# Kernel optimization log

Measured on AMD Instinct MI355X. Metric: run time of the kernel, lower is better.

The kernel has to match this reference:

```python
import jax, jax.numpy as jnp
import numpy as np


def setup_inputs() -> dict:
    key = jax.random.key(0)
    k1, k2 = jax.random.split(key)
    z = jax.random.normal(k1, (16, 256, 4096), dtype=jnp.float32)  # (B, z_dim, T)
    embedding = jax.random.normal(k2, (1024, 256), dtype=jnp.float32)  # (z_num, z_dim)
    return {"z": z, "embedding": embedding}


def reference(z, embedding):
    # z: (B, C, T) -> (B, T, C), matching z.transpose(1, 2)
    zt = jnp.transpose(z, (0, 2, 1))
    B, T, C = zt.shape
    z_flat = zt.reshape(-1, C)  # (N, C), N = B*T

    # squared-euclidean distances: ||z||^2 + ||e||^2 - 2 z e^T  -> (N, K)
    distances = (
        jnp.sum(z_flat * z_flat, axis=1, keepdims=True)
        + jnp.sum(embedding * embedding, axis=1)
        - 2.0 * z_flat @ embedding.T
    )
    encoding_idx = jnp.argmin(distances, axis=1)  # (N,)
    z_vq = embedding[encoding_idx].reshape(B, T, C)

    # perplexity of code usage (one-hot scatter -> mean)
    K = embedding.shape[0]
    counts = jnp.zeros((K,), dtype=jnp.float32).at[encoding_idx].add(1.0)
    avg_probs = counts / encoding_idx.shape[0]
    perplexity = jnp.exp(-jnp.sum(avg_probs * jnp.log(avg_probs + 1e-10)))

    # sparsity = cross_entropy(E E^T, arange) = mean(logsumexp(row) - diag)
    logits = embedding @ embedding.T  # (K, K)
    sparsity = jnp.mean(jax.nn.logsumexp(logits, axis=1) - jnp.diag(logits))

    sg = jax.lax.stop_gradient
    z_qut_loss = jnp.sum((z_vq - sg(zt)) ** 2)   # mse_loss reduction='sum'
    z_enc_loss = jnp.sum((sg(z_vq) - zt) ** 2)

    # straight-through estimator
    z_st = zt + sg(z_vq - zt)
    out = jnp.transpose(z_st, (0, 2, 1))  # back to (B, C, T)
    return (out, z_qut_loss, z_enc_loss, perplexity, sparsity)
```

## Files before the change

kernel.cpp:

```cpp
#include <hip/hip_runtime.h>
#include <math.h>

typedef unsigned int u32;
typedef unsigned long long u64;
typedef _Float16 f16x8 __attribute__((ext_vector_type(8)));
typedef _Float16 f16x4 __attribute__((ext_vector_type(4)));
typedef float f32x4 __attribute__((ext_vector_type(4)));
typedef __attribute__((address_space(1))) const char gch;
typedef __attribute__((address_space(3))) char lch;

#define ZD 256
#define KC 1024
#define TT 4096
#define BB 16
#define NROWS (BB*TT)
#define TAU 0.12f
#define FLAGCAP 32768

__device__ __forceinline__ u32 flip32(float s) {
    int i = __float_as_int(s);
    return (u32)(i ^ ((i >> 31) | 0x80000000));
}
__device__ __forceinline__ float unflip32(u32 u) {
    int m = (~(((int)u) >> 31)) | 0x80000000;
    return __int_as_float((int)(u ^ (u32)m));
}

__global__ __launch_bounds__(256)
void vq_prep_kernel(const float* __restrict__ emb, _Float16* __restrict__ eh,
                    float* __restrict__ re, int* __restrict__ cnt) {
    int gid = blockIdx.x * 256 + threadIdx.x;
    if (gid < 2) cnt[gid] = 0;

    int code = gid >> 6;
    int lane = threadIdx.x & 63;
    float4 v = *(const float4*)(emb + (size_t)code * ZD + lane * 4);
    float s = v.x*v.x + v.y*v.y + v.z*v.z + v.w*v.w;
    #pragma unroll
    for (int off = 32; off; off >>= 1) s += __shfl_down(s, off, 64);
    if (lane == 0) re[code] = s;

    f16x4 hv;
    hv[0] = (_Float16)v.x; hv[1] = (_Float16)v.y;
    hv[2] = (_Float16)v.z; hv[3] = (_Float16)v.w;
    *(f16x4*)(eh + (size_t)code * ZD + lane * 4) = hv;
}

__device__ __forceinline__ void stage_half4(const char* ehc, char* dstbase,
                                            int h, int w, int l) {
    const int srow = h * 16384;
    #pragma unroll
    for (int j = 0; j < 4; ++j) {
        const int gi  = w * 4 + j;
        const int c   = 2 * gi + (l >> 5);
        const int kbs = (l & 31) * 16;
        const int off = srow + c * 512 + (kbs ^ ((c & 7) << 4));
        __builtin_amdgcn_global_load_lds((gch*)(ehc + off),
                                         (lch*)(dstbase + gi * 1024), 16, 0, 0);
    }
}

__device__ __forceinline__ void compute_phase32(const char* hb, int h,
                                                const f16x8 (&ah)[2][8], const float* reL,
                                                float (&v1)[8], float (&v2)[8], int (&i1)[8],
                                                int lane15, int lk) {
    #pragma unroll
    for (int cg = 0; cg < 2; ++cg) {
        const int c  = cg * 16 + lane15;
        const int sw = (lane15 & 7) << 4;
        f16x8 bh[8];
        #pragma unroll
        for (int ks = 0; ks < 8; ++ks)
            bh[ks] = *(const f16x8*)(hb + c * 512 + ((lk * 16 + ks * 64) ^ sw));

        f32x4 a0 = {0.f, 0.f, 0.f, 0.f};
        f32x4 a1 = {0.f, 0.f, 0.f, 0.f};
        __builtin_amdgcn_s_setprio(1);
        #pragma unroll
        for (int ks = 0; ks < 8; ++ks) {
            a0 = __builtin_amdgcn_mfma_f32_16x16x32_f16(ah[0][ks], bh[ks], a0, 0, 0, 0);
            a1 = __builtin_amdgcn_mfma_f32_16x16x32_f16(ah[1][ks], bh[ks], a1, 0, 0, 0);
        }
        __builtin_amdgcn_s_setprio(0);

        const int codeg = h * 32 + c;
        const float rc = reL[codeg];
        #pragma unroll
        for (int r = 0; r < 4; ++r) {
            float s0 = fmaf(-2.f, a0[r], rc);
            float n2a = fminf(fmaxf(v1[r], s0), v2[r]);
            i1[r] = (s0 < v1[r]) ? codeg : i1[r];
            v1[r] = fminf(v1[r], s0);
            v2[r] = n2a;
            float s1 = fmaf(-2.f, a1[r], rc);
            float n2b = fminf(fmaxf(v1[4 + r], s1), v2[4 + r]);
            i1[4 + r] = (s1 < v1[4 + r]) ? codeg : i1[4 + r];
            v1[4 + r] = fminf(v1[4 + r], s1);
            v2[4 + r] = n2b;
        }
    }
}

__global__ __launch_bounds__(256, 3)
void vq_argmin_mfma(const float* __restrict__ z, const _Float16* __restrict__ eh,
                    const float* __restrict__ emb, const float* __restrict__ re,
                    float* __restrict__ out, float* __restrict__ lossP,
                    int* __restrict__ idx, int* __restrict__ cnt,
                    int* __restrict__ flags) {
    __shared__ __align__(16) char lds[53248];
    float* reL    = (float*)(lds + 49152);
    int*   idsL   = (int*)lds;
    float* wlossL = (float*)(lds + 512);

    const int tid = threadIdx.x;
    const int w   = tid >> 6;
    const int l   = tid & 63;
    const int lane15 = l & 15;
    const int lk     = l >> 4;
    const int r0  = blockIdx.x * 128;
    const int b   = r0 >> 12;
    const int t0  = r0 & 4095;
    const char* ehc = (const char*)eh;

    *(float4*)(reL + tid * 4) = *(const float4*)(re + tid * 4);

    f16x8 ah[2][8];
    float zsq[2] = {0.f, 0.f};
    {
        const char* zb = (const char*)(z + (size_t)b * ZD * TT + t0 + w * 32);
        char* zdst = lds + w * 8192;
        #pragma unroll
        for (int round = 0; round < 4; ++round) {
            #pragma unroll
            for (int j = 0; j < 8; ++j) {
                const int c  = round * 64 + j * 8 + (l >> 3);
                const int tb = (l & 7) * 16;
                const char* src = zb + (size_t)c * TT * 4 + tb;
                __builtin_amdgcn_global_load_lds((gch*)src, (lch*)(zdst + j * 1024),
                                                 16, 0, 0);
            }
            asm volatile("s_waitcnt vmcnt(0)" ::: "memory");
            __builtin_amdgcn_sched_barrier(0);
            #pragma unroll
            for (int rg = 0; rg < 2; ++rg) {
                const int tw = rg * 16 + lane15;
                #pragma unroll
                for (int ks2 = 0; ks2 < 2; ++ks2) {
                    const int cl = ks2 * 32 + lk * 8;
                    f16x8 h;
                    #pragma unroll
                    for (int j = 0; j < 8; ++j) {
                        float v = *(const float*)(zdst + (cl + j) * 128 + tw * 4);
                        zsq[rg] = fmaf(v, v, zsq[rg]);
                        h[j] = (_Float16)v;
                    }
                    ah[rg][round * 2 + ks2] = h;
                }
            }
            asm volatile("s_waitcnt lgkmcnt(0)" ::: "memory");
            __builtin_amdgcn_sched_barrier(0);
        }
    }
    #pragma unroll
    for (int rg = 0; rg < 2; ++rg) {
        zsq[rg] += __shfl_xor(zsq[rg], 16, 64);
        zsq[rg] += __shfl_xor(zsq[rg], 32, 64);
    }

    float v1[8], v2[8];
    int   i1[8];
    #pragma unroll
    for (int s8 = 0; s8 < 8; ++s8) { v1[s8] = 3.4e38f; v2[s8] = 3.4e38f; i1[s8] = 0; }

    asm volatile("s_waitcnt vmcnt(0) lgkmcnt(0)" ::: "memory");
    __syncthreads();
    stage_half4(ehc, lds,         0, w, l);
    stage_half4(ehc, lds + 16384, 1, w, l);

    for (int h = 0; h < 31; ++h) {
        asm volatile("s_waitcnt vmcnt(4)" ::: "memory");
        __builtin_amdgcn_sched_barrier(0);
        __builtin_amdgcn_s_barrier();
        if (h < 30) stage_half4(ehc, lds + ((h + 2) % 3) * 16384, h + 2, w, l);
        compute_phase32(lds + (h % 3) * 16384, h, ah, reL, v1, v2, i1, lane15, lk);
    }
    asm volatile("s_waitcnt vmcnt(0)" ::: "memory");
    __builtin_amdgcn_sched_barrier(0);
    __builtin_amdgcn_s_barrier();
    compute_phase32(lds + (31 % 3) * 16384, 31, ah, reL, v1, v2, i1, lane15, lk);

    #pragma unroll
    for (int off = 1; off < 16; off <<= 1) {
        #pragma unroll
        for (int s8 = 0; s8 < 8; ++s8) {
            float ov1 = __shfl_xor(v1[s8], off, 64);
            int   oi1 = __shfl_xor(i1[s8], off, 64);
            float ov2 = __shfl_xor(v2[s8], off, 64);
            float nv2 = fminf(fmaxf(v1[s8], ov1), fminf(v2[s8], ov2));
            if (ov1 < v1[s8] || (ov1 == v1[s8] && oi1 < i1[s8])) { v1[s8] = ov1; i1[s8] = oi1; }
            v2[s8] = nv2;
        }
    }

    float zsr[8];
    #pragma unroll
    for (int s8 = 0; s8 < 8; ++s8) {
        const int rg = s8 >> 2, rr = s8 & 3;
        zsr[s8] = __shfl(zsq[rg], lk * 4 + rr, 64);
    }

    __syncthreads();
    float lossw = 0.f;
    if (lane15 == 0) {
        #pragma unroll
        for (int s8 = 0; s8 < 8; ++s8) {
            const int rg = s8 >> 2, rr = s8 & 3;
            const int row = w * 32 + rg * 16 + lk * 4 + rr;
            idsL[row] = i1[s8];
            const bool fl = (v2[s8] - v1[s8] < TAU);
            lossw += fl ? zsr[s8] : (zsr[s8] + v1[s8]);
            if (fl) {
                int p = atomicAdd(cnt, 1);
                if (p < FLAGCAP) flags[p] = (r0 + row) | (i1[s8] << 16);
            }
        }
    }
    lossw += __shfl_xor(lossw, 16, 64);
    lossw += __shfl_xor(lossw, 32, 64);
    if (l == 0) wlossL[w] = lossw;
    __syncthreads();

    if (tid < 128) idx[r0 + tid] = idsL[tid];
    if (tid == 0) lossP[blockIdx.x] = wlossL[0] + wlossL[1] + wlossL[2] + wlossL[3];

    {
        const int c0 = w * 64;
        float* ob = out + (size_t)b * ZD * TT + t0;
        #pragma unroll
        for (int half = 0; half < 2; ++half) {
            const int tt = half * 64 + l;
            const int ii = idsL[tt];
            const float4* er4 = (const float4*)(emb + (size_t)ii * ZD + c0);
            #pragma unroll
            for (int c4 = 0; c4 < 16; ++c4) {
                float4 ev = er4[c4];
                float* o0 = ob + (size_t)(c0 + c4 * 4) * TT + tt;
                o0[0]      = ev.x;
                o0[TT]     = ev.y;
                o0[2 * TT] = ev.z;
                o0[3 * TT] = ev.w;
            }
        }
    }
}

__global__ __launch_bounds__(256)
void vq_fixup_spar(const float* __restrict__ z, const float* __restrict__ emb,
                   const float* __restrict__ re, const int* __restrict__ cnt,
                   const int* __restrict__ flags, float* __restrict__ out,
                   int* __restrict__ idx, float* __restrict__ spar,
                   float* __restrict__ addP) {
    const int tid = threadIdx.x;
    const int w   = tid >> 6;
    const int lane = tid & 63;

    if (blockIdx.x >= 128) {
        __shared__ __align__(16) float er[8][260];
        __shared__ float wmaxS[8][4];
        __shared__ float wsumS[8][4];
        __shared__ float shD[8];
        const int bid2 = blockIdx.x - 128;
        const int r0   = bid2 * 8;

        for (int i = tid; i < 8 * 256; i += 256) er[i >> 8][i & 255] = emb[(size_t)r0 * ZD + i];
        __syncthreads();

        float dots[4][8];
        #pragma unroll
        for (int cc = 0; cc < 4; ++cc) {
            const int c = cc * 256 + tid;
            const float4* ec = (const float4*)(emb + (size_t)c * ZD);
            float a[8] = {0.f,0.f,0.f,0.f,0.f,0.f,0.f,0.f};
            for (int k4 = 0; k4 < ZD / 4; ++k4) {
                float4 e4 = ec[k4];
                #pragma unroll
                for (int r = 0; r < 8; ++r) {
                    const float* a4 = &er[r][k4 * 4];
                    a[r] = fmaf(e4.x, a4[0], fmaf(e4.y, a4[1],
                           fmaf(e4.z, a4[2], fmaf(e4.w, a4[3], a[r]))));
                }
            }
            #pragma unroll
            for (int r = 0; r < 8; ++r) dots[cc][r] = a[r];
            const int gr = c - r0;
            if (gr >= 0 && gr < 8) shD[gr] = a[gr];
        }
        #pragma unroll
        for (int r = 0; r < 8; ++r) {
            float m = fmaxf(fmaxf(dots[0][r], dots[1][r]), fmaxf(dots[2][r], dots[3][r]));
            #pragma unroll
            for (int off = 32; off; off >>= 1) m = fmaxf(m, __shfl_xor(m, off, 64));
            if (lane == 0) wmaxS[r][w] = m;
        }
        __syncthreads();
        #pragma unroll
        for (int r = 0; r < 8; ++r) {
            const float M = fmaxf(fmaxf(wmaxS[r][0], wmaxS[r][1]),
                                  fmaxf(wmaxS[r][2], wmaxS[r][3]));
            float se = expf(dots[0][r] - M) + expf(dots[1][r] - M)
                     + expf(dots[2][r] - M) + expf(dots[3][r] - M);
            #pragma unroll
            for (int off = 32; off; off >>= 1) se += __shfl_xor(se, off, 64);
            if (lane == 0) wsumS[r][w] = se;
        }
        __syncthreads();
        if (tid == 0) {
            float acc = 0.f;
            #pragma unroll
            for (int r = 0; r < 8; ++r) {
                const float M = fmaxf(fmaxf(wmaxS[r][0], wmaxS[r][1]),
                                      fmaxf(wmaxS[r][2], wmaxS[r][3]));
                const float S = wsumS[r][0] + wsumS[r][1] + wsumS[r][2] + wsumS[r][3];
                acc += M + logf(S) - shD[r];
            }
            spar[bid2] = acc;
        }
        return;
    }

    __shared__ __align__(16) float zs[8][ZD];
    __shared__ u64 sb[4][8];
    __shared__ int nwS[8];
    __shared__ float addS;
    int n = cnt[0];
    if (n > FLAGCAP) n = FLAGCAP;
    float blkLoss = 0.f;

    for (int base = blockIdx.x * 8; base < n; base += 128 * 8) {
        const int nr = (n - base < 8) ? (n - base) : 8;
        __syncthreads();
        for (int i = tid; i < nr * 256; i += 256) {
            const int r = i >> 8, k = i & 255;
            const int rowg = flags[base + r] & 0xFFFF;
            zs[r][k] = z[(size_t)(rowg >> 12) * ZD * TT + (size_t)k * TT + (rowg & 4095)];
        }
        __syncthreads();

        u64 best[8];
        #pragma unroll
        for (int r = 0; r < 8; ++r) best[r] = 0xFFFFFFFFFFFFFFFFull;

        for (int cc = 0; cc < 4; ++cc) {
            const int c = cc * 256 + tid;
            const float4* ec = (const float4*)(emb + (size_t)c * ZD);
            float a[8] = {0.f,0.f,0.f,0.f,0.f,0.f,0.f,0.f};
            for (int k4 = 0; k4 < ZD / 4; ++k4) {
                float4 e4 = ec[k4];
                #pragma unroll
                for (int r = 0; r < 8; ++r) {
                    const float* a4 = &zs[r][k4 * 4];
                    a[r] = fmaf(e4.x, a4[0], fmaf(e4.y, a4[1],
                           fmaf(e4.z, a4[2], fmaf(e4.w, a4[3], a[r]))));
                }
            }
            const float rc = re[c];
            #pragma unroll
            for (int r = 0; r < 8; ++r) {
                if (r < nr) {
                    float s = fmaf(-2.f, a[r], rc);
                    u64 pk = ((u64)flip32(s) << 32) | (u32)c;
                    if (pk < best[r]) best[r] = pk;
                }
            }
        }
        #pragma unroll
        for (int r = 0; r < 8; ++r) {
            if (r < nr) {
                u64 bv = best[r];
                #pragma unroll
                for (int off = 32; off; off >>= 1) {
                    u64 o = (u64)__shfl_xor((long long)bv, off, 64);
                    if (o < bv) bv = o;
                }
                if (lane == 0) sb[w][r] = bv;
            }
        }
        __syncthreads();
        if (tid == 0) addS = 0.f;
        __syncthreads();
        if (tid < nr) {
            u64 m = sb[0][tid];
            if (sb[1][tid] < m) m = sb[1][tid];
            if (sb[2][tid] < m) m = sb[2][tid];
            if (sb[3][tid] < m) m = sb[3][tid];
            const int nc  = (int)(u32)(m & 0xFFFFFFFFull);
            const float s = unflip32((u32)(m >> 32));
            const int rowg = flags[base + tid] & 0xFFFF;
            const int old  = (flags[base + tid] >> 16) & 1023;
            atomicAdd(&addS, s);
            if (nc != old) { idx[rowg] = nc; nwS[tid] = nc; }
            else nwS[tid] = -1;
        }
        __syncthreads();
        if (tid == 0) blkLoss += addS;
        for (int r = 0; r < nr; ++r) {
            const int nw = nwS[r];
            if (nw >= 0) {
                const int rowg = flags[base + r] & 0xFFFF;
                out[(size_t)(rowg >> 12) * ZD * TT + (size_t)tid * TT + (rowg & 4095)]
                    = emb[(size_t)nw * ZD + tid];
            }
        }
    }
    if (tid == 0) addP[blockIdx.x] = blkLoss;
}

__global__ __launch_bounds__(1024)
void vq_final_kernel(const int* __restrict__ idx, const float* __restrict__ spar,
                     const float* __restrict__ lossP, const float* __restrict__ addP,
                     float* __restrict__ scal) {
    __shared__ int   histL[4][1024];
    __shared__ float red[1024];
    const int tid = threadIdx.x;
    const int g   = tid >> 8;

    histL[0][tid] = 0; histL[1][tid] = 0; histL[2][tid] = 0; histL[3][tid] = 0;
    __syncthreads();
    #pragma unroll 4
    for (int i = 0; i < 64; ++i)
        atomicAdd(&histL[g][idx[i * 1024 + tid]], 1);
    __syncthreads();
    const int hc = histL[0][tid] + histL[1][tid] + histL[2][tid] + histL[3][tid];
    float p = (float)hc * (1.0f / (float)NROWS);
    red[tid] = -p * logf(p + 1e-10f);
    __syncthreads();
    for (int st = 512; st; st >>= 1) {
        if (tid < st) red[tid] += red[tid + st];
        __syncthreads();
    }
    if (tid == 0) scal[2] = expf(red[0]);
    __syncthreads();

    red[tid] = (tid < 512 ? lossP[tid] : 0.f) + ((tid < 128) ? addP[tid] : 0.f);
    __syncthreads();
    for (int st = 512; st; st >>= 1) {
        if (tid < st) red[tid] += red[tid + st];
        __syncthreads();
    }
    if (tid == 0) { scal[0] = red[0]; scal[1] = red[0]; }
    __syncthreads();

    red[tid] = (tid < 128) ? spar[tid] : 0.f;
    __syncthreads();
    for (int st = 512; st; st >>= 1) {
        if (tid < st) red[tid] += red[tid + st];
        __syncthreads();
    }
    if (tid == 0) scal[3] = red[0] * (1.0f / (float)KC);
}

extern "C" void kernel_launch(void* const* d_in, const int* in_sizes, int n_in,
                              void* d_out, int out_size, void* d_ws, size_t ws_size,
                              hipStream_t stream) {
    const float* z   = (const float*)d_in[0];
    const float* emb = (const float*)d_in[1];
    float* out = (float*)d_out;
    const size_t NOUT = (size_t)BB * ZD * TT;
    float* scal = out + NOUT;

    float* re    = (float*)d_ws;
    int*   cnt   = (int*)(re + KC);
    int*   flags = cnt + 4;
    float* spar  = (float*)(flags + FLAGCAP);
    float* lossP = spar + 128;
    float* addP  = lossP + 512;
    int*   idx   = (int*)(addP + 128);
    _Float16* eh = (_Float16*)(idx + NROWS);

    vq_prep_kernel<<<256, 256, 0, stream>>>(emb, eh, re, cnt);
    vq_argmin_mfma<<<NROWS / 128, 256, 0, stream>>>(z, eh, emb, re, out, lossP, idx,
                                                    cnt, flags);
    vq_fixup_spar<<<256, 256, 0, stream>>>(z, emb, re, cnt, flags, out, idx, spar, addP);
    vq_final_kernel<<<1, 1024, 0, stream>>>(idx, spar, lossP, addP, scal);
}
```

Before: 172.8 us.

## Double argmin block to 512 threads with 16 rows per wave

The argmin kernel now launches 512 threads per block. Each wave owns 16 rows instead of 32, and each MFMA chain splits K into even and odd accumulators. Code staging per thread is halved, and the per-wave register state (A fragments, top-2 trackers) shrinks. This is meant to raise wave occupancy and latency hiding. In exchange, each code tile loaded into LDS is reused by fewer rows per wave, and more waves contend at every barrier.

After: 172.0 us. No clear change (-0.4%).

```diff
diff --git a/kernel.cpp b/kernel.cpp
--- a/kernel.cpp
+++ b/kernel.cpp
@@ -46,12 +46,12 @@
     *(f16x4*)(eh + (size_t)code * ZD + lane * 4) = hv;
 }
 
-__device__ __forceinline__ void stage_half4(const char* ehc, char* dstbase,
+__device__ __forceinline__ void stage_half8(const char* ehc, char* dstbase,
                                             int h, int w, int l) {
     const int srow = h * 16384;
     #pragma unroll
-    for (int j = 0; j < 4; ++j) {
-        const int gi  = w * 4 + j;
+    for (int j = 0; j < 2; ++j) {
+        const int gi  = w * 2 + j;
         const int c   = 2 * gi + (l >> 5);
         const int kbs = (l & 31) * 16;
         const int off = srow + c * 512 + (kbs ^ ((c & 7) << 4));
@@ -60,9 +60,9 @@
     }
 }
 
-__device__ __forceinline__ void compute_phase32(const char* hb, int h,
-                                                const f16x8 (&ah)[2][8], const float* reL,
-                                                float (&v1)[8], float (&v2)[8], int (&i1)[8],
+__device__ __forceinline__ void compute_phase16(const char* hb, int h,
+                                                const f16x8 (&ah)[8], const float* reL,
+                                                float (&v1)[4], float (&v2)[4], int (&i1)[4],
                                                 int lane15, int lk) {
     #pragma unroll
     for (int cg = 0; cg < 2; ++cg) {
@@ -73,13 +73,13 @@
         for (int ks = 0; ks < 8; ++ks)
             bh[ks] = *(const f16x8*)(hb + c * 512 + ((lk * 16 + ks * 64) ^ sw));
 
-        f32x4 a0 = {0.f, 0.f, 0.f, 0.f};
-        f32x4 a1 = {0.f, 0.f, 0.f, 0.f};
+        f32x4 ae = {0.f, 0.f, 0.f, 0.f};
+        f32x4 ao = {0.f, 0.f, 0.f, 0.f};
         __builtin_amdgcn_s_setprio(1);
         #pragma unroll
-        for (int ks = 0; ks < 8; ++ks) {
-            a0 = __builtin_amdgcn_mfma_f32_16x16x32_f16(ah[0][ks], bh[ks], a0, 0, 0, 0);
-            a1 = __builtin_amdgcn_mfma_f32_16x16x32_f16(ah[1][ks], bh[ks], a1, 0, 0, 0);
+        for (int ks = 0; ks < 4; ++ks) {
+            ae = __builtin_amdgcn_mfma_f32_16x16x32_f16(ah[2 * ks],     bh[2 * ks],     ae, 0, 0, 0);
+            ao = __builtin_amdgcn_mfma_f32_16x16x32_f16(ah[2 * ks + 1], bh[2 * ks + 1], ao, 0, 0, 0);
         }
         __builtin_amdgcn_s_setprio(0);
 
@@ -87,21 +87,16 @@
         const float rc = reL[codeg];
         #pragma unroll
         for (int r = 0; r < 4; ++r) {
-            float s0 = fmaf(-2.f, a0[r], rc);
-            float n2a = fminf(fmaxf(v1[r], s0), v2[r]);
+            float s0 = fmaf(-2.f, ae[r] + ao[r], rc);
+            float n2 = fminf(fmaxf(v1[r], s0), v2[r]);
             i1[r] = (s0 < v1[r]) ? codeg : i1[r];
             v1[r] = fminf(v1[r], s0);
-            v2[r] = n2a;
-            float s1 = fmaf(-2.f, a1[r], rc);
-            float n2b = fminf(fmaxf(v1[4 + r], s1), v2[4 + r]);
-            i1[4 + r] = (s1 < v1[4 + r]) ? codeg : i1[4 + r];
-            v1[4 + r] = fminf(v1[4 + r], s1);
-            v2[4 + r] = n2b;
-        }
-    }
-}
-
-__global__ __launch_bounds__(256, 3)
+            v2[r] = n2;
+        }
+    }
+}
+
+__global__ __launch_bounds__(512, 4)
 void vq_argmin_mfma(const float* __restrict__ z, const _Float16* __restrict__ eh,
                     const float* __restrict__ emb, const float* __restrict__ re,
                     float* __restrict__ out, float* __restrict__ lossP,
@@ -110,7 +105,7 @@
     __shared__ __align__(16) char lds[53248];
     float* reL    = (float*)(lds + 49152);
     int*   idsL   = (int*)lds;
-    float* wlossL = (float*)(lds + 512);
+    float* wlossL = (float*)(lds + 1024);
 
     const int tid = threadIdx.x;
     const int w   = tid >> 6;
@@ -122,19 +117,20 @@
     const int t0  = r0 & 4095;
     const char* ehc = (const char*)eh;
 
-    *(float4*)(reL + tid * 4) = *(const float4*)(re + tid * 4);
-
-    f16x8 ah[2][8];
-    float zsq[2] = {0.f, 0.f};
+    *(float2*)(reL + tid * 2) = *(const float2*)(re + tid * 2);
+
+    f16x8 ah[8];
+    float zsq = 0.f;
     {
-        const char* zb = (const char*)(z + (size_t)b * ZD * TT + t0 + w * 32);
-        char* zdst = lds + w * 8192;
+        const char* zb = (const char*)(z + (size_t)b * ZD * TT + t0 + w * 16);
+        char* zdst = lds + w * 4096;
         #pragma unroll
         for (int round = 0; round < 4; ++round) {
             #pragma unroll
-            for (int j = 0; j < 8; ++j) {
-                const int c  = round * 64 + j * 8 + (l >> 3);
-                const int tb = (l & 7) * 16;
+            for (int j = 0; j < 4; ++j) {
+                const int cl = j * 16 + (l >> 2);
+                const int tb = (l & 3) * 16;
+                const int c  = round * 64 + cl;
                 const char* src = zb + (size_t)c * TT * 4 + tb;
                 __builtin_amdgcn_global_load_lds((gch*)src, (lch*)(zdst + j * 1024),
                                                  16, 0, 0);
@@ -142,86 +138,75 @@
             asm volatile("s_waitcnt vmcnt(0)" ::: "memory");
             __builtin_amdgcn_sched_barrier(0);
             #pragma unroll
-            for (int rg = 0; rg < 2; ++rg) {
-                const int tw = rg * 16 + lane15;
+            for (int ks2 = 0; ks2 < 2; ++ks2) {
+                const int cl0 = ks2 * 32 + lk * 8;
+                f16x8 h;
                 #pragma unroll
-                for (int ks2 = 0; ks2 < 2; ++ks2) {
-                    const int cl = ks2 * 32 + lk * 8;
-                    f16x8 h;
-                    #pragma unroll
-                    for (int j = 0; j < 8; ++j) {
-                        float v = *(const float*)(zdst + (cl + j) * 128 + tw * 4);
-                        zsq[rg] = fmaf(v, v, zsq[rg]);
-                        h[j] = (_Float16)v;
-                    }
-                    ah[rg][round * 2 + ks2] = h;
+                for (int j = 0; j < 8; ++j) {
+                    float v = *(const float*)(zdst + (cl0 + j) * 64 + lane15 * 4);
+                    zsq = fmaf(v, v, zsq);
+                    h[j] = (_Float16)v;
                 }
+                ah[round * 2 + ks2] = h;
             }
             asm volatile("s_waitcnt lgkmcnt(0)" ::: "memory");
             __builtin_amdgcn_sched_barrier(0);
         }
     }
-    #pragma unroll
-    for (int rg = 0; rg < 2; ++rg) {
-        zsq[rg] += __shfl_xor(zsq[rg], 16, 64);
-        zsq[rg] += __shfl_xor(zsq[rg], 32, 64);
-    }
-
-    float v1[8], v2[8];
-    int   i1[8];
-    #pragma unroll
-    for (int s8 = 0; s8 < 8; ++s8) { v1[s8] = 3.4e38f; v2[s8] = 3.4e38f; i1[s8] = 0; }
+    zsq += __shfl_xor(zsq, 16, 64);
+    zsq += __shfl_xor(zsq, 32, 64);
+
+    float v1[4], v2[4];
+    int   i1[4];
+    #pragma unroll
+    for (int r = 0; r < 4; ++r) { v1[r] = 3.4e38f; v2[r] = 3.4e38f; i1[r] = 0; }
 
     asm volatile("s_waitcnt vmcnt(0) lgkmcnt(0)" ::: "memory");
     __syncthreads();
-    stage_half4(ehc, lds,         0, w, l);
-    stage_half4(ehc, lds + 16384, 1, w, l);
+    stage_half8(ehc, lds,         0, w, l);
+    stage_half8(ehc, lds + 16384, 1, w, l);
 
     for (int h = 0; h < 31; ++h) {
-        asm volatile("s_waitcnt vmcnt(4)" ::: "memory");
+        asm volatile("s_waitcnt vmcnt(2)" ::: "memory");
         __builtin_amdgcn_sched_barrier(0);
         __builtin_amdgcn_s_barrier();
-        if (h < 30) stage_half4(ehc, lds + ((h + 2) % 3) * 16384, h + 2, w, l);
-        compute_phase32(lds + (h % 3) * 16384, h, ah, reL, v1, v2, i1, lane15, lk);
+        if (h < 30) stage_half8(ehc, lds + ((h + 2) % 3) * 16384, h + 2, w, l);
+        compute_phase16(lds + (h % 3) * 16384, h, ah, reL, v1, v2, i1, lane15, lk);
     }
     asm volatile("s_waitcnt vmcnt(0)" ::: "memory");
     __builtin_amdgcn_sched_barrier(0);
     __builtin_amdgcn_s_barrier();
-    compute_phase32(lds + (31 % 3) * 16384, 31, ah, reL, v1, v2, i1, lane15, lk);
+    compute_phase16(lds + (31 % 3) * 16384, 31, ah, reL, v1, v2, i1, lane15, lk);
 
     #pragma unroll
     for (int off = 1; off < 16; off <<= 1) {
         #pragma unroll
-        for (int s8 = 0; s8 < 8; ++s8) {
-            float ov1 = __shfl_xor(v1[s8], off, 64);
-            int   oi1 = __shfl_xor(i1[s8], off, 64);
-            float ov2 = __shfl_xor(v2[s8], off, 64);
-            float nv2 = fminf(fmaxf(v1[s8], ov1), fminf(v2[s8], ov2));
-            if (ov1 < v1[s8] || (ov1 == v1[s8] && oi1 < i1[s8])) { v1[s8] = ov1; i1[s8] = oi1; }
-            v2[s8] = nv2;
-        }
-    }
-
-    float zsr[8];
-    #pragma unroll
-    for (int s8 = 0; s8 < 8; ++s8) {
-        const int rg = s8 >> 2, rr = s8 & 3;
-        zsr[s8] = __shfl(zsq[rg], lk * 4 + rr, 64);
-    }
+        for (int r = 0; r < 4; ++r) {
+            float ov1 = __shfl_xor(v1[r], off, 64);
+            int   oi1 = __shfl_xor(i1[r], off, 64);
+            float ov2 = __shfl_xor(v2[r], off, 64);
+            float nv2 = fminf(fmaxf(v1[r], ov1), fminf(v2[r], ov2));
+            if (ov1 < v1[r] || (ov1 == v1[r] && oi1 < i1[r])) { v1[r] = ov1; i1[r] = oi1; }
+            v2[r] = nv2;
+        }
+    }
+
+    float zsr[4];
+    #pragma unroll
+    for (int r = 0; r < 4; ++r) zsr[r] = __shfl(zsq, lk * 4 + r, 64);
 
     __syncthreads();
     float lossw = 0.f;
     if (lane15 == 0) {
         #pragma unroll
-        for (int s8 = 0; s8 < 8; ++s8) {
-            const int rg = s8 >> 2, rr = s8 & 3;
-            const int row = w * 32 + rg * 16 + lk * 4 + rr;
-            idsL[row] = i1[s8];
-            const bool fl = (v2[s8] - v1[s8] < TAU);
-            lossw += fl ? zsr[s8] : (zsr[s8] + v1[s8]);
+        for (int r = 0; r < 4; ++r) {
+            const int row = w * 16 + lk * 4 + r;
+            idsL[row] = i1[r];
+            const bool fl = (v2[r] - v1[r] < TAU);
+            lossw += fl ? zsr[r] : (zsr[r] + v1[r]);
             if (fl) {
                 int p = atomicAdd(cnt, 1);
-                if (p < FLAGCAP) flags[p] = (r0 + row) | (i1[s8] << 16);
+                if (p < FLAGCAP) flags[p] = (r0 + row) | (i1[r] << 16);
             }
         }
     }
@@ -231,10 +216,15 @@
     __syncthreads();
 
     if (tid < 128) idx[r0 + tid] = idsL[tid];
-    if (tid == 0) lossP[blockIdx.x] = wlossL[0] + wlossL[1] + wlossL[2] + wlossL[3];
+    if (tid == 0) {
+        float s = 0.f;
+        #pragma unroll
+        for (int j = 0; j < 8; ++j) s += wlossL[j];
+        lossP[blockIdx.x] = s;
+    }
 
     {
-        const int c0 = w * 64;
+        const int c0 = w * 32;
         float* ob = out + (size_t)b * ZD * TT + t0;
         #pragma unroll
         for (int half = 0; half < 2; ++half) {
@@ -242,7 +232,7 @@
             const int ii = idsL[tt];
             const float4* er4 = (const float4*)(emb + (size_t)ii * ZD + c0);
             #pragma unroll
-            for (int c4 = 0; c4 < 16; ++c4) {
+            for (int c4 = 0; c4 < 8; ++c4) {
                 float4 ev = er4[c4];
                 float* o0 = ob + (size_t)(c0 + c4 * 4) * TT + tt;
                 o0[0]      = ev.x;
@@ -478,7 +468,7 @@
     _Float16* eh = (_Float16*)(idx + NROWS);
 
     vq_prep_kernel<<<256, 256, 0, stream>>>(emb, eh, re, cnt);
-    vq_argmin_mfma<<<NROWS / 128, 256, 0, stream>>>(z, eh, emb, re, out, lossP, idx,
+    vq_argmin_mfma<<<NROWS / 128, 512, 0, stream>>>(z, eh, emb, re, out, lossP, idx,
                                                     cnt, flags);
     vq_fixup_spar<<<256, 256, 0, stream>>>(z, emb, re, cnt, flags, out, idx, spar, addP);
     vq_final_kernel<<<1, 1024, 0, stream>>>(idx, spar, lossP, addP, scal);
```
